# Optimization experiments

Measured on AMD Instinct MI355X. Metric: run time of the kernel, lower is better.

## Reference

```python
import jax, jax.numpy as jnp
import numpy as np

NUM_HEADS = 16
EMB_SIZE = 1024
HEAD_SIZE = 64


def setup_inputs() -> dict:
    key = jax.random.key(0)
    ks = jax.random.split(key, 9)
    H, E, D = NUM_HEADS, EMB_SIZE, HEAD_SIZE
    s = 1.0 / np.sqrt(E)
    X = jax.random.normal(ks[0], (4, 2048, E), dtype=jnp.float32)
    Wq = jax.random.uniform(ks[1], (H, E, D), jnp.float32, -s, s)
    Wk = jax.random.uniform(ks[2], (H, E, D), jnp.float32, -s, s)
    Wv = jax.random.uniform(ks[3], (H, E, D), jnp.float32, -s, s)
    bq = jax.random.uniform(ks[4], (H, D), jnp.float32, -s, s)
    bk = jax.random.uniform(ks[5], (H, D), jnp.float32, -s, s)
    bv = jax.random.uniform(ks[6], (H, D), jnp.float32, -s, s)
    so = 1.0 / np.sqrt(H * D)
    Wo = jax.random.uniform(ks[7], (H * D, E), jnp.float32, -so, so)
    bo = jax.random.uniform(ks[8], (E,), jnp.float32, -so, so)
    return {"X": X, "Wq": Wq, "Wk": Wk, "Wv": Wv, "bq": bq, "bk": bk, "bv": bv, "Wo": Wo, "bo": bo}


def reference(X, Wq, Wk, Wv, bq, bk, bv, Wo, bo):
    B, S, E = X.shape
    H, _, D = Wq.shape
    # per-head projections (batched over heads)
    q = jnp.einsum('bse,hed->bhsd', X, Wq) + bq[None, :, None, :]
    k = jnp.einsum('bse,hed->bhsd', X, Wk) + bk[None, :, None, :]
    v = jnp.einsum('bse,hed->bhsd', X, Wv) + bv[None, :, None, :]
    # causal scaled-dot-product attention
    scores = jnp.einsum('bhsd,bhtd->bhst', q, k) / jnp.sqrt(jnp.float32(D))
    causal = jnp.tril(jnp.ones((S, S), dtype=bool))
    scores = jnp.where(causal[None, None], scores, jnp.float32(-jnp.inf))
    probs = jax.nn.softmax(scores, axis=-1)
    out = jnp.einsum('bhst,bhtd->bhsd', probs, v)
    # concat heads (head h occupies slots [h*D:(h+1)*D]) then output proj
    concat = out.transpose(0, 2, 1, 3).reshape(B, S, H * D)
    # dropout is identity in eval mode
    return concat @ Wo + bo
```

## Files before the change

kernel.cpp:

```cpp
#include <hip/hip_runtime.h>
#include <stdint.h>


typedef float   f32x4  __attribute__((ext_vector_type(4)));
typedef __bf16  bf16x8 __attribute__((ext_vector_type(8)));
typedef short   short8 __attribute__((ext_vector_type(8)));
typedef unsigned short ushort4v __attribute__((ext_vector_type(4)));

typedef __attribute__((address_space(1))) void GV;
typedef __attribute__((address_space(3))) void LV;

#define DEVI static __device__ __forceinline__

DEVI unsigned short f2bf(float f){
  unsigned u = __float_as_uint(f);
  unsigned r = u + 0x7fffu + ((u>>16)&1u);
  return (unsigned short)(r>>16);
}

DEVI unsigned cvt_pk_bf16(float lo, float hi){
  unsigned r;
  asm("v_cvt_pk_bf16_f32 %0, %1, %2" : "=v"(r) : "v"(lo), "v"(hi));
  return r;
}

DEVI void gl_lds16(const void* g, void* l){
  __builtin_amdgcn_global_load_lds((GV*)g, (LV*)l, 16, 0, 0);
}

__global__ __launch_bounds__(256) void pack_x(const float* __restrict__ X,
                                              short* __restrict__ Xb){
  int i = blockIdx.x*256 + threadIdx.x;
  const float4* p = (const float4*)(X + (size_t)i*8);
  float4 a = p[0], b = p[1];
  short8 o;
  o[0]=(short)f2bf(a.x); o[1]=(short)f2bf(a.y); o[2]=(short)f2bf(a.z); o[3]=(short)f2bf(a.w);
  o[4]=(short)f2bf(b.x); o[5]=(short)f2bf(b.y); o[6]=(short)f2bf(b.z); o[7]=(short)f2bf(b.w);
  *(short8*)(Xb + (size_t)i*8) = o;
}

__global__ __launch_bounds__(256) void pack_wqkv(const float* __restrict__ Wq,
                                                 const float* __restrict__ Wk,
                                                 const float* __restrict__ Wv,
                                                 short* __restrict__ Wp){
  int t = blockIdx.x*256 + threadIdx.x;
  int n = t >> 7, kc = t & 127;
  int which = n >> 10, hd = n & 1023, h = hd >> 6, d = hd & 63;
  const float* W = which==0 ? Wq : (which==1 ? Wk : Wv);
  const float* src = W + ((size_t)h*1024 + kc*8)*64 + d;
  short8 o;
  #pragma unroll
  for (int j=0;j<8;++j) o[j] = (short)f2bf(src[(size_t)j*64]);
  *(short8*)(Wp + (size_t)n*1024 + kc*8) = o;
}

__global__ __launch_bounds__(256) void pack_wo(const float* __restrict__ Wo,
                                               short* __restrict__ WoT){
  int t = blockIdx.x*256 + threadIdx.x;
  int n = t >> 7, kc = t & 127;
  const float* src = Wo + (size_t)(kc*8)*1024 + n;
  short8 o;
  #pragma unroll
  for (int j=0;j<8;++j) o[j] = (short)f2bf(src[(size_t)j*1024]);
  *(short8*)(WoT + (size_t)n*1024 + kc*8) = o;
}

template<int MODE>
__global__ __launch_bounds__(256)
void gemm128(const short* __restrict__ A, const short* __restrict__ Bt,
             const float* __restrict__ b0, const float* __restrict__ b1,
             const float* __restrict__ b2,
             short* __restrict__ Qb, short* __restrict__ Kb, short* __restrict__ Vtb,
             float* __restrict__ Out)
{
  __shared__ __align__(16) char smA[128*128];
  __shared__ __align__(16) char smB[128*128];
  const int K2 = 2048;
  int t = threadIdx.x, lane = t & 63, wid = t >> 6;
  int wr = wid >> 1, wc = wid & 1;
  int l15 = lane & 15, l4 = lane >> 4;
  int nwg = gridDim.x, qd = nwg >> 3;
  int swz = (blockIdx.x & 7) * qd + (blockIdx.x >> 3);
  int bm = swz & 63, bn = swz >> 6;
  size_t abase = (size_t)bm * 128 * K2;
  size_t bbase = (size_t)bn * 128 * K2;

  f32x4 acc[4][4] = {};

  for (int kt = 0; kt < 16; ++kt){
    int kb = kt * 128;
    #pragma unroll
    for (int c = 0; c < 4; ++c){
      int x = c*4096 + t*16;
      int r = x >> 7, z = x & 127;
      int zs = z ^ ((r & 7) << 4);
      gl_lds16((const char*)A  + abase + (size_t)r*K2 + kb + zs, smA + c*4096 + wid*1024);
      gl_lds16((const char*)Bt + bbase + (size_t)r*K2 + kb + zs, smB + c*4096 + wid*1024);
    }
    __syncthreads();
    #pragma unroll
    for (int kk = 0; kk < 2; ++kk){
      bf16x8 af[4], bfr[4];
      int cb = kk*64 + l4*16;
      #pragma unroll
      for (int i = 0; i < 4; ++i){
        int ra = wr*64 + i*16 + l15;
        af[i]  = *(const bf16x8*)(smA + ra*128 + (cb ^ ((ra&7)<<4)));
        int rb = wc*64 + i*16 + l15;
        bfr[i] = *(const bf16x8*)(smB + rb*128 + (cb ^ ((rb&7)<<4)));
      }
      __builtin_amdgcn_s_setprio(1);
      #pragma unroll
      for (int i = 0; i < 4; ++i)
        #pragma unroll
        for (int j = 0; j < 4; ++j)
          acc[i][j] = __builtin_amdgcn_mfma_f32_16x16x32_bf16(af[i], bfr[j], acc[i][j], 0, 0, 0);
      __builtin_amdgcn_s_setprio(0);
    }
    __syncthreads();
  }

  #pragma unroll
  for (int i = 0; i < 4; ++i){
    int mbase = bm*128 + wr*64 + i*16 + l4*4;
    #pragma unroll
    for (int j = 0; j < 4; ++j){
      int n = bn*128 + wc*64 + j*16 + l15;
      if (MODE == 0){
        int which = n >> 10, hd = n & 1023, h = hd >> 6, d = hd & 63;
        const float* bp = which==0 ? b0 : (which==1 ? b1 : b2);
        float bias = bp[hd];
        int b = mbase >> 11, sbase = mbase & 2047;
        size_t bh = (size_t)(b*16 + h);
        if (which == 2){
          ushort4v pv;
          #pragma unroll
          for (int r = 0; r < 4; ++r) pv[r] = f2bf(acc[i][j][r] + bias);
          *(ushort4v*)(Vtb + (bh*64 + d)*2048 + sbase) = pv;
        } else {
          short* dst = (which==0 ? Qb : Kb) + bh*2048*64;
          float sc = which==0 ? 0.18033688f : 1.0f;
          #pragma unroll
          for (int r = 0; r < 4; ++r)
            dst[(size_t)(sbase + r)*64 + d] = (short)f2bf((acc[i][j][r] + bias) * sc);
        }
      } else {
        float bias = b0[n];
        #pragma unroll
        for (int r = 0; r < 4; ++r)
          Out[(size_t)(mbase + r)*1024 + n] = acc[i][j][r] + bias;
      }
    }
  }
}

__global__ __launch_bounds__(256, 4)
void attn(const short* __restrict__ Qb, const short* __restrict__ Kb,
          const short* __restrict__ Vtb, short* __restrict__ Ob)
{
  __shared__ __align__(16) char smK[2][8192];
  __shared__ __align__(16) char smV[2][8192];
  __shared__ __align__(16) char smP[4][2048];
  int t = threadIdx.x, lane = t & 63, wid = t >> 6;
  int l15 = lane & 15, hi = lane >> 4;
  int hi16 = hi*16, hi4 = hi*4;
  int bh = blockIdx.x & 63;
  int j = blockIdx.x >> 6;
  int qb = (j < 8) ? (15 - j) : (j - 8);
  int b = bh >> 4, h = bh & 15;
  int q0 = qb * 128;
  int wq0 = q0 + wid * 32;
  const char* Qh = (const char*)(Qb + (size_t)bh*2048*64);
  const char* Kh = (const char*)(Kb + (size_t)bh*2048*64);
  const char* Vh = (const char*)(Vtb + (size_t)bh*64*2048);
  char* Pw = smP[wid];

  bf16x8 qf[2][2];
  #pragma unroll
  for (int qt = 0; qt < 2; ++qt)
    #pragma unroll
    for (int kk = 0; kk < 2; ++kk)
      qf[qt][kk] = *(const bf16x8*)(Qh + (size_t)(wq0 + qt*16 + l15)*128 + kk*64 + hi16);

  f32x4 oacc[2][4] = {};
  float m[2] = {-1e30f, -1e30f}, l[2] = {0.f, 0.f};

  int nkt = 2*qb + 2;

  #pragma unroll
  for (int c = 0; c < 2; ++c){
    int x = c*4096 + t*16;
    int r = x >> 7, z = x & 127;
    int zs = z ^ ((r & 7) << 4);
    gl_lds16(Kh + (size_t)r*128 + zs, smK[0] + c*4096 + wid*1024);
    gl_lds16(Vh + (size_t)r*4096 + zs, smV[0] + c*4096 + wid*1024);
  }
  __syncthreads();

  for (int kt = 0; kt < nkt; ++kt){
    int cur = kt & 1;
    if (kt + 1 < nkt){
      int nxt = cur ^ 1;
      #pragma unroll
      for (int c = 0; c < 2; ++c){
        int x = c*4096 + t*16;
        int r = x >> 7, z = x & 127;
        int zs = z ^ ((r & 7) << 4);
        gl_lds16(Kh + (size_t)(kt+1)*8192 + (size_t)r*128 + zs, smK[nxt] + c*4096 + wid*1024);
        gl_lds16(Vh + (size_t)r*4096 + (size_t)(kt+1)*128 + zs, smV[nxt] + c*4096 + wid*1024);
      }
    }
    const char* Kc = smK[cur];
    const char* Vc = smV[cur];
    int kbase = kt * 64;

    #pragma unroll
    for (int qt = 0; qt < 2; ++qt){
      int qlo = wq0 + qt*16;
      if (kbase > qlo + 15) continue;

      f32x4 sa[4];
      __builtin_amdgcn_s_setprio(1);
      #pragma unroll
      for (int nt = 0; nt < 4; ++nt){
        f32x4 a = {};
        #pragma unroll
        for (int kk = 0; kk < 2; ++kk){
          int rk = nt*16 + l15;
          bf16x8 kf = *(const bf16x8*)(Kc + rk*128 + ((kk*64 + hi16) ^ ((rk&7)<<4)));
          a = __builtin_amdgcn_mfma_f32_16x16x32_bf16(kf, qf[qt][kk], a, 0, 0, 0);
        }
        sa[nt] = a;
      }
      __builtin_amdgcn_s_setprio(0);

      int qrow = qlo + l15;
      if (kbase + 63 > qlo){
        #pragma unroll
        for (int nt = 0; nt < 4; ++nt)
          #pragma unroll
          for (int r = 0; r < 4; ++r)
            if (kbase + nt*16 + hi4 + r > qrow) sa[nt][r] = -1e30f;
      }

      float pm = sa[0][0];
      #pragma unroll
      for (int nt = 0; nt < 4; ++nt)
        #pragma unroll
        for (int r = 0; r < 4; ++r) pm = fmaxf(pm, sa[nt][r]);
      pm = fmaxf(pm, __shfl_xor(pm, 16));
      pm = fmaxf(pm, __shfl_xor(pm, 32));
      float mq = m[qt];
      if (!__all(pm <= mq + 8.0f)){
        float mnew = fmaxf(mq, pm);
        float sc = exp2f(mq - mnew);
        l[qt] *= sc;
        #pragma unroll
        for (int dt = 0; dt < 4; ++dt) oacc[qt][dt] *= sc;
        m[qt] = mnew; mq = mnew;
      }
      float rs = 0.f;
      unsigned pw[8];
      #pragma unroll
      for (int nt = 0; nt < 4; ++nt){
        float p0 = exp2f(sa[nt][0] - mq);
        float p1 = exp2f(sa[nt][1] - mq);
        float p2 = exp2f(sa[nt][2] - mq);
        float p3 = exp2f(sa[nt][3] - mq);
        rs += (p0 + p1) + (p2 + p3);
        pw[nt*2]   = cvt_pk_bf16(p0, p1);
        pw[nt*2+1] = cvt_pk_bf16(p2, p3);
      }
      rs += __shfl_xor(rs, 16);
      rs += __shfl_xor(rs, 32);
      l[qt] += rs;

      {
        char* base = Pw + l15*128;
        int sw = (l15 & 7) << 4;
        #pragma unroll
        for (int nt = 0; nt < 4; ++nt){
          unsigned long long w = (unsigned long long)pw[nt*2] |
                                 ((unsigned long long)pw[nt*2+1] << 32);
          *(unsigned long long*)(base + ((nt*32 + hi*8) ^ sw)) = w;
        }
      }

      __builtin_amdgcn_s_setprio(1);
      #pragma unroll
      for (int kk = 0; kk < 2; ++kk){
        bf16x8 pf = *(const bf16x8*)(Pw + l15*128 + ((kk*64 + hi16) ^ ((l15&7)<<4)));
        #pragma unroll
        for (int dt = 0; dt < 4; ++dt){
          int rv = dt*16 + l15;
          bf16x8 vf = *(const bf16x8*)(Vc + rv*128 + ((kk*64 + hi16) ^ ((rv&7)<<4)));
          oacc[qt][dt] = __builtin_amdgcn_mfma_f32_16x16x32_bf16(vf, pf, oacc[qt][dt], 0, 0, 0);
        }
      }
      __builtin_amdgcn_s_setprio(0);
    }
    __syncthreads();
  }

  #pragma unroll
  for (int qt = 0; qt < 2; ++qt){
    float inv = 1.0f / l[qt];
    int srow = wq0 + qt*16 + l15;
    size_t rb = ((size_t)(b*2048 + srow))*1024 + h*64 + hi4;
    #pragma unroll
    for (int dt = 0; dt < 4; ++dt){
      unsigned w0 = cvt_pk_bf16(oacc[qt][dt][0]*inv, oacc[qt][dt][1]*inv);
      unsigned w1 = cvt_pk_bf16(oacc[qt][dt][2]*inv, oacc[qt][dt][3]*inv);
      *(unsigned long long*)(Ob + rb + dt*16) =
          ((unsigned long long)w1 << 32) | (unsigned long long)w0;
    }
  }
}

extern "C" void kernel_launch(void* const* d_in, const int* in_sizes, int n_in,
                              void* d_out, int out_size, void* d_ws, size_t ws_size,
                              hipStream_t stream)
{
  const float* X  = (const float*)d_in[0];
  const float* Wq = (const float*)d_in[1];
  const float* Wk = (const float*)d_in[2];
  const float* Wv = (const float*)d_in[3];
  const float* bq = (const float*)d_in[4];
  const float* bk = (const float*)d_in[5];
  const float* bv = (const float*)d_in[6];
  const float* Wo = (const float*)d_in[7];
  const float* bo = (const float*)d_in[8];
  float* Out = (float*)d_out;

  char* ws = (char*)d_ws;
  short* Xbf  = (short*)(ws);
  short* Wp   = (short*)(ws + 16777216);
  short* WoT  = (short*)(ws + 23068672);
  short* Qb   = (short*)(ws + 25165824);
  short* Kb   = (short*)(ws + 41943040);
  short* Vtb  = (short*)(ws + 58720256);
  short* Ob   = (short*)(ws + 75497472);

  pack_x   <<<4096, 256, 0, stream>>>(X, Xbf);
  pack_wqkv<<<1536, 256, 0, stream>>>(Wq, Wk, Wv, Wp);
  pack_wo  <<< 512, 256, 0, stream>>>(Wo, WoT);

  gemm128<0><<<24*64, 256, 0, stream>>>(Xbf, Wp, bq, bk, bv, Qb, Kb, Vtb, nullptr);
  attn      <<<64*16, 256, 0, stream>>>(Qb, Kb, Vtb, Ob);
  gemm128<1><<< 8*64, 256, 0, stream>>>(Ob, WoT, bo, nullptr, nullptr,
                                        nullptr, nullptr, nullptr, Out);
}
```

Measured before the change: 219.0 us.

## Widen GEMM tiles with triple-buffered LDS pipeline; compute softmax row sums via MFMA

The GEMM kernel moves to a 128x256 tile with 512 threads and a three-stage LDS ring. The next-next K tile is prefetched while the current one computes, using explicit vmcnt waits and barriers, and this replaces the load-then-sync loop. The attention kernel drops the per-tile shuffle reduction of row sums and gets them from an extra MFMA of the P tile against a ones vector. The max reduction is also rebalanced into a shallower tree. The cost is 144KB of LDS per block, which allows only one block per CU, plus hand-tuned waitcnt values that must match the issued load count exactly.

Result: faster. 204.5 us (-6.6%).

```diff
diff --git a/kernel.cpp b/kernel.cpp
--- a/kernel.cpp
+++ b/kernel.cpp
@@ -66,38 +66,47 @@
 }
 
 template<int MODE>
-__global__ __launch_bounds__(256)
-void gemm128(const short* __restrict__ A, const short* __restrict__ Bt,
+__global__ __launch_bounds__(512)
+void gemm256(const short* __restrict__ A, const short* __restrict__ Bt,
              const float* __restrict__ b0, const float* __restrict__ b1,
              const float* __restrict__ b2,
              short* __restrict__ Qb, short* __restrict__ Kb, short* __restrict__ Vtb,
              float* __restrict__ Out)
 {
-  __shared__ __align__(16) char smA[128*128];
-  __shared__ __align__(16) char smB[128*128];
+  __shared__ __align__(16) char sm[3][49152];
   const int K2 = 2048;
   int t = threadIdx.x, lane = t & 63, wid = t >> 6;
-  int wr = wid >> 1, wc = wid & 1;
+  int wr = wid >> 2, wc = wid & 3;
   int l15 = lane & 15, l4 = lane >> 4;
   int nwg = gridDim.x, qd = nwg >> 3;
   int swz = (blockIdx.x & 7) * qd + (blockIdx.x >> 3);
   int bm = swz & 63, bn = swz >> 6;
   size_t abase = (size_t)bm * 128 * K2;
-  size_t bbase = (size_t)bn * 128 * K2;
+  size_t bbase = (size_t)bn * 256 * K2;
 
   f32x4 acc[4][4] = {};
 
-  for (int kt = 0; kt < 16; ++kt){
+  auto stage = [&](int kt, char* buf){
     int kb = kt * 128;
     #pragma unroll
-    for (int c = 0; c < 4; ++c){
-      int x = c*4096 + t*16;
+    for (int c = 0; c < 2; ++c){
+      int x = c*8192 + t*16;
       int r = x >> 7, z = x & 127;
       int zs = z ^ ((r & 7) << 4);
-      gl_lds16((const char*)A  + abase + (size_t)r*K2 + kb + zs, smA + c*4096 + wid*1024);
-      gl_lds16((const char*)Bt + bbase + (size_t)r*K2 + kb + zs, smB + c*4096 + wid*1024);
-    }
-    __syncthreads();
+      gl_lds16((const char*)A + abase + (size_t)r*K2 + kb + zs, buf + c*8192 + wid*1024);
+    }
+    #pragma unroll
+    for (int c = 0; c < 4; ++c){
+      int x = c*8192 + t*16;
+      int r = x >> 7, z = x & 127;
+      int zs = z ^ ((r & 7) << 4);
+      gl_lds16((const char*)Bt + bbase + (size_t)r*K2 + kb + zs, buf + 16384 + c*8192 + wid*1024);
+    }
+  };
+
+  auto compute = [&](const char* buf){
+    const char* sA = buf;
+    const char* sB = buf + 16384;
     #pragma unroll
     for (int kk = 0; kk < 2; ++kk){
       bf16x8 af[4], bfr[4];
@@ -105,9 +114,9 @@
       #pragma unroll
       for (int i = 0; i < 4; ++i){
         int ra = wr*64 + i*16 + l15;
-        af[i]  = *(const bf16x8*)(smA + ra*128 + (cb ^ ((ra&7)<<4)));
+        af[i]  = *(const bf16x8*)(sA + ra*128 + (cb ^ ((ra&7)<<4)));
         int rb = wc*64 + i*16 + l15;
-        bfr[i] = *(const bf16x8*)(smB + rb*128 + (cb ^ ((rb&7)<<4)));
+        bfr[i] = *(const bf16x8*)(sB + rb*128 + (cb ^ ((rb&7)<<4)));
       }
       __builtin_amdgcn_s_setprio(1);
       #pragma unroll
@@ -117,15 +126,27 @@
           acc[i][j] = __builtin_amdgcn_mfma_f32_16x16x32_bf16(af[i], bfr[j], acc[i][j], 0, 0, 0);
       __builtin_amdgcn_s_setprio(0);
     }
-    __syncthreads();
-  }
+  };
+
+  stage(0, sm[0]);
+  stage(1, sm[1]);
+  for (int kt = 0; kt < 14; ++kt){
+    stage(kt + 2, sm[(kt + 2) % 3]);
+    asm volatile("s_waitcnt vmcnt(12)\n\ts_barrier" ::: "memory");
+    compute(sm[kt % 3]);
+    asm volatile("s_barrier" ::: "memory");
+  }
+  asm volatile("s_waitcnt vmcnt(6)\n\ts_barrier" ::: "memory");
+  compute(sm[2]);
+  asm volatile("s_waitcnt vmcnt(0)" ::: "memory");
+  compute(sm[0]);
 
   #pragma unroll
   for (int i = 0; i < 4; ++i){
     int mbase = bm*128 + wr*64 + i*16 + l4*4;
     #pragma unroll
     for (int j = 0; j < 4; ++j){
-      int n = bn*128 + wc*64 + j*16 + l15;
+      int n = bn*256 + wc*64 + j*16 + l15;
       if (MODE == 0){
         int which = n >> 10, hd = n & 1023, h = hd >> 6, d = hd & 63;
         const float* bp = which==0 ? b0 : (which==1 ? b1 : b2);
@@ -175,6 +196,10 @@
   const char* Vh = (const char*)(Vtb + (size_t)bh*64*2048);
   char* Pw = smP[wid];
 
+  bf16x8 vones;
+  #pragma unroll
+  for (int z = 0; z < 8; ++z) vones[z] = (__bf16)1.0f;
+
   bf16x8 qf[2][2];
   #pragma unroll
   for (int qt = 0; qt < 2; ++qt)
@@ -183,7 +208,8 @@
       qf[qt][kk] = *(const bf16x8*)(Qh + (size_t)(wq0 + qt*16 + l15)*128 + kk*64 + hi16);
 
   f32x4 oacc[2][4] = {};
-  float m[2] = {-1e30f, -1e30f}, l[2] = {0.f, 0.f};
+  f32x4 lacc[2] = {};
+  float m[2] = {-1e30f, -1e30f};
 
   int nkt = 2*qb + 2;
 
@@ -243,23 +269,28 @@
             if (kbase + nt*16 + hi4 + r > qrow) sa[nt][r] = -1e30f;
       }
 
-      float pm = sa[0][0];
-      #pragma unroll
-      for (int nt = 0; nt < 4; ++nt)
-        #pragma unroll
-        for (int r = 0; r < 4; ++r) pm = fmaxf(pm, sa[nt][r]);
+      float pm;
+      {
+        float t0 = fmaxf(fmaxf(sa[0][0], sa[0][1]), sa[0][2]);
+        float t1 = fmaxf(fmaxf(sa[0][3], sa[1][0]), sa[1][1]);
+        float t2 = fmaxf(fmaxf(sa[1][2], sa[1][3]), sa[2][0]);
+        float t3 = fmaxf(fmaxf(sa[2][1], sa[2][2]), sa[2][3]);
+        float t4 = fmaxf(fmaxf(sa[3][0], sa[3][1]), sa[3][2]);
+        float u0 = fmaxf(fmaxf(t0, t1), sa[3][3]);
+        float u1 = fmaxf(fmaxf(t2, t3), t4);
+        pm = fmaxf(u0, u1);
+      }
       pm = fmaxf(pm, __shfl_xor(pm, 16));
       pm = fmaxf(pm, __shfl_xor(pm, 32));
       float mq = m[qt];
       if (!__all(pm <= mq + 8.0f)){
         float mnew = fmaxf(mq, pm);
         float sc = exp2f(mq - mnew);
-        l[qt] *= sc;
+        lacc[qt] *= sc;
         #pragma unroll
         for (int dt = 0; dt < 4; ++dt) oacc[qt][dt] *= sc;
         m[qt] = mnew; mq = mnew;
       }
-      float rs = 0.f;
       unsigned pw[8];
       #pragma unroll
       for (int nt = 0; nt < 4; ++nt){
@@ -267,13 +298,9 @@
         float p1 = exp2f(sa[nt][1] - mq);
         float p2 = exp2f(sa[nt][2] - mq);
         float p3 = exp2f(sa[nt][3] - mq);
-        rs += (p0 + p1) + (p2 + p3);
         pw[nt*2]   = cvt_pk_bf16(p0, p1);
         pw[nt*2+1] = cvt_pk_bf16(p2, p3);
       }
-      rs += __shfl_xor(rs, 16);
-      rs += __shfl_xor(rs, 32);
-      l[qt] += rs;
 
       {
         char* base = Pw + l15*128;
@@ -290,6 +317,7 @@
       #pragma unroll
       for (int kk = 0; kk < 2; ++kk){
         bf16x8 pf = *(const bf16x8*)(Pw + l15*128 + ((kk*64 + hi16) ^ ((l15&7)<<4)));
+        lacc[qt] = __builtin_amdgcn_mfma_f32_16x16x32_bf16(vones, pf, lacc[qt], 0, 0, 0);
         #pragma unroll
         for (int dt = 0; dt < 4; ++dt){
           int rv = dt*16 + l15;
@@ -304,7 +332,7 @@
 
   #pragma unroll
   for (int qt = 0; qt < 2; ++qt){
-    float inv = 1.0f / l[qt];
+    float inv = 1.0f / lacc[qt][0];
     int srow = wq0 + qt*16 + l15;
     size_t rb = ((size_t)(b*2048 + srow))*1024 + h*64 + hi4;
     #pragma unroll
@@ -345,8 +373,8 @@
   pack_wqkv<<<1536, 256, 0, stream>>>(Wq, Wk, Wv, Wp);
   pack_wo  <<< 512, 256, 0, stream>>>(Wo, WoT);
 
-  gemm128<0><<<24*64, 256, 0, stream>>>(Xbf, Wp, bq, bk, bv, Qb, Kb, Vtb, nullptr);
+  gemm256<0><<<768, 512, 0, stream>>>(Xbf, Wp, bq, bk, bv, Qb, Kb, Vtb, nullptr);
   attn      <<<64*16, 256, 0, stream>>>(Qb, Kb, Vtb, Ob);
-  gemm128<1><<< 8*64, 256, 0, stream>>>(Ob, WoT, bo, nullptr, nullptr,
-                                        nullptr, nullptr, nullptr, Out);
-}
+  gemm256<1><<<256, 512, 0, stream>>>(Ob, WoT, bo, nullptr, nullptr,
+                                      nullptr, nullptr, nullptr, Out);
+}
```
